# Optimization experiments

Measured on AMD Instinct MI355X. Metric: run time of the kernel, lower is better.

## Reference

```python
import jax, jax.numpy as jnp
import numpy as np

EPS = 1e-08
SINKHORN_ITERS = 5
SINKHORN_TAU = 0.05


def l2_normalize(x, axis=-1):
    return x / (jnp.linalg.norm(x, axis=axis, keepdims=True) + EPS)


def sinkhorn_balanced(logits, iters=SINKHORN_ITERS, tau=SINKHORN_TAU):
    # logits: [B, N, K]
    b, n, k = logits.shape
    q = jnp.exp(logits / tau)
    q = q / (jnp.sum(q, axis=(1, 2), keepdims=True) + EPS)
    target_row = 1.0 / float(n)
    target_col = 1.0 / float(k)
    for _ in range(iters):
        q = q / (jnp.sum(q, axis=2, keepdims=True) + EPS) * target_row
        q = q / (jnp.sum(q, axis=1, keepdims=True) + EPS) * target_col
    q = q / (jnp.sum(q, axis=2, keepdims=True) + EPS)
    return q


def assign(x, proto):
    x_n = l2_normalize(x)          # [B,N,D]
    p_n = l2_normalize(proto)      # [K,D]
    sim = jnp.einsum('bnd,kd->bnk', x_n, p_n)
    a = sinkhorn_balanced(sim)
    z_rec = jnp.einsum('bnk,kd->bnd', a, p_n)
    return z_rec, a, sim


def setup_inputs() -> dict:
    key = jax.random.key(0)
    k1, k2, k3, k4 = jax.random.split(key, 4)
    B, N, D, K = 16, 1024, 256, 256
    return {
        'f_rgb': jax.random.normal(k1, (B, N, D), dtype=jnp.float32),
        'f_sn': jax.random.normal(k2, (B, N, D), dtype=jnp.float32),
        'proto_rgb': jax.random.normal(k3, (K, D), dtype=jnp.float32) * 0.02,
        'proto_sn': jax.random.normal(k4, (K, D), dtype=jnp.float32) * 0.02,
    }


def reference(f_rgb, f_sn, proto_rgb, proto_sn):
    z_rgb, assign_rgb, sim_rgb = assign(f_rgb, proto_rgb)
    z_sn, assign_sn, sim_sn = assign(f_sn, proto_sn)
    # cross-modal consistency maps: [B,N,N]
    rgb_to_sn = jnp.matmul(assign_rgb, jnp.swapaxes(assign_sn, -1, -2))
    sn_to_rgb = jnp.matmul(assign_sn, jnp.swapaxes(assign_rgb, -1, -2))
    sem_consistency = 0.5 * (
        1.0 - jnp.clip(jnp.mean(rgb_to_sn), 0.0, 1.0)
        + 1.0 - jnp.clip(jnp.mean(sn_to_rgb), 0.0, 1.0)
    )
    return (z_rgb, z_sn, assign_rgb, assign_sn, sim_rgb, sim_sn, sem_consistency)
```

## Files before the change

### kernel.cpp

```cpp
#include <hip/hip_runtime.h>
#include <hip/hip_bf16.h>
#include <cstdint>
#include <cstddef>

#define EPS 1e-8f

typedef __attribute__((ext_vector_type(8))) short short8;
typedef __attribute__((ext_vector_type(4))) float floatx4;

static constexpr int Bb = 16, Nn = 1024, Dd = 256, Kk = 256;
static constexpr int M = Bb * Nn;
static constexpr size_t PM = (size_t)M * 256;

static constexpr size_t OUT_Z      = 0;
static constexpr size_t OUT_ASSIGN = 2 * PM;
static constexpr size_t OUT_SIM    = 4 * PM;
static constexpr size_t OUT_SEM    = 6 * PM;

static constexpr size_t OFF_XN  = 0;
static constexpr size_t OFF_QB  = 16777216;
static constexpr size_t OFF_PN  = 33554432;
static constexpr size_t OFF_PNT = 33816576;
static constexpr size_t OFF_U   = 34078720;
static constexpr size_t OFF_T   = 34209792;
static constexpr size_t OFF_SC  = 34209920;
static constexpr size_t OFF_CS  = 34406528;
static constexpr size_t ZERO_OFF = OFF_T;
static constexpr size_t ZERO_SZ  = 128 + 196608 + 32768;
static constexpr int    NZ_FLOATS = (int)(ZERO_SZ / 4);

__device__ __forceinline__ unsigned short f2bf(float f) {
    unsigned int b = __float_as_uint(f);
    b += 0x7fffu + ((b >> 16) & 1u);
    return (unsigned short)(b >> 16);
}
__device__ __forceinline__ float bf2f(unsigned short u) {
    return __uint_as_float(((unsigned int)u) << 16);
}

typedef const __attribute__((address_space(1))) unsigned int* gas_u32p;
typedef __attribute__((address_space(3))) unsigned int* las_u32p;
__device__ __forceinline__ void lds_cp16(const unsigned short* g, short* l) {
    __builtin_amdgcn_global_load_lds((gas_u32p)g, (las_u32p)l, 16, 0, 0);
}

__global__ __launch_bounds__(256) void prep_kernel(const float* __restrict__ fr,
                                                   const float* __restrict__ fs,
                                                   unsigned short* __restrict__ xn) {
    int mod = blockIdx.y;
    int row = blockIdx.x * 4 + (threadIdx.x >> 6);
    int lane = threadIdx.x & 63;
    const float* src = (mod ? fs : fr) + (size_t)row * 256;
    float4 v = ((const float4*)src)[lane];
    float ss = v.x * v.x + v.y * v.y + v.z * v.z + v.w * v.w;
    #pragma unroll
    for (int m = 1; m < 64; m <<= 1) ss += __shfl_xor(ss, m);
    float sc = 1.0f / (sqrtf(ss) + EPS);
    ushort4 u4;
    u4.x = f2bf(v.x * sc); u4.y = f2bf(v.y * sc);
    u4.z = f2bf(v.z * sc); u4.w = f2bf(v.w * sc);
    *(ushort4*)(xn + (size_t)mod * PM + (size_t)row * 256 + lane * 4) = u4;
}

__global__ __launch_bounds__(64) void proto_kernel(const float* __restrict__ pr,
                                                   const float* __restrict__ ps,
                                                   unsigned short* __restrict__ pn,
                                                   unsigned short* __restrict__ pnt,
                                                   float* __restrict__ zp) {
    int gid = blockIdx.x * 64 + threadIdx.x;
    for (int i = gid; i < NZ_FLOATS; i += 32768) zp[i] = 0.f;

    int row = blockIdx.x & 255;
    int mod = blockIdx.x >> 8;
    const float* p = (mod ? ps : pr) + (size_t)row * 256;
    int lane = threadIdx.x;
    float4 v = ((const float4*)p)[lane];
    float ss = v.x * v.x + v.y * v.y + v.z * v.z + v.w * v.w;
    #pragma unroll
    for (int m = 1; m < 64; m <<= 1) ss += __shfl_xor(ss, m);
    float sc = 1.0f / (sqrtf(ss) + EPS);
    ushort4 u4;
    u4.x = f2bf(v.x * sc); u4.y = f2bf(v.y * sc);
    u4.z = f2bf(v.z * sc); u4.w = f2bf(v.w * sc);
    *(ushort4*)(pn + (size_t)mod * 65536 + (size_t)row * 256 + lane * 4) = u4;
    unsigned short* pt = pnt + (size_t)mod * 65536 + row;
    pt[(size_t)(lane * 4 + 0) * 256] = u4.x;
    pt[(size_t)(lane * 4 + 1) * 256] = u4.y;
    pt[(size_t)(lane * 4 + 2) * 256] = u4.z;
    pt[(size_t)(lane * 4 + 3) * 256] = u4.w;
}

template <int MODE>
__global__ __launch_bounds__(256) void gemm_kernel(const unsigned short* __restrict__ Asrc,
                                                   const unsigned short* __restrict__ Bsrc,
                                                   unsigned short* __restrict__ qb,
                                                   float* __restrict__ doutf,
                                                   float* __restrict__ Tg) {
    __shared__ short Al[8192];
    __shared__ short Bl[8192];

    int bx = blockIdx.x;
    int by = blockIdx.y;
    int mod = blockIdx.z;
    int t = threadIdx.x;
    int lane = t & 63, wv = t >> 6;
    int wrow = (wv >> 1) * 64, wcol = (wv & 1) * 64;
    int g = lane >> 4, ml = lane & 15;

    const unsigned short* A0 = Asrc + (size_t)mod * PM + (size_t)by * 128 * 256;
    const unsigned short* B0 = Bsrc + (size_t)mod * 65536 + (size_t)bx * 128 * 256;

    floatx4 acc[4][4];
    #pragma unroll
    for (int i = 0; i < 4; i++)
        #pragma unroll
        for (int j = 0; j < 4; j++) acc[i][j] = (floatx4){0.f, 0.f, 0.f, 0.f};

    for (int kh = 0; kh < 4; kh++) {
        #pragma unroll
        for (int i = 0; i < 4; i++) {
            int sI = i * 256 + t;
            int r = sI >> 3, cs = sI & 7;
            int cg = cs ^ (r & 7);
            size_t goff = (size_t)r * 256 + kh * 64 + cg * 8;
            lds_cp16(A0 + goff, &Al[sI * 8]);
            lds_cp16(B0 + goff, &Bl[sI * 8]);
        }
        __syncthreads();
        #pragma unroll
        for (int ks = 0; ks < 2; ks++) {
            short8 af[4], bfr[4];
            int c = ks * 4 + g;
            #pragma unroll
            for (int mt = 0; mt < 4; mt++) {
                int row = wrow + mt * 16 + ml;
                af[mt] = *(const short8*)&Al[row * 64 + (c ^ (row & 7)) * 8];
            }
            #pragma unroll
            for (int nt = 0; nt < 4; nt++) {
                int row = wcol + nt * 16 + ml;
                bfr[nt] = *(const short8*)&Bl[row * 64 + (c ^ (row & 7)) * 8];
            }
            #pragma unroll
            for (int mt = 0; mt < 4; mt++)
                #pragma unroll
                for (int nt = 0; nt < 4; nt++)
                    acc[mt][nt] = __builtin_amdgcn_mfma_f32_16x16x32_bf16(af[mt], bfr[nt], acc[mt][nt], 0, 0, 0);
        }
        __syncthreads();
    }

    int g4 = g << 2;
    float tsum = 0.f;
    #pragma unroll
    for (int mt = 0; mt < 4; mt++)
        #pragma unroll
        for (int nt = 0; nt < 4; nt++)
            #pragma unroll
            for (int reg = 0; reg < 4; reg++) {
                float s = acc[mt][nt][reg];
                int row = by * 128 + wrow + mt * 16 + g4 + reg;
                int col = bx * 128 + wcol + nt * 16 + ml;
                size_t idx = (size_t)row * 256 + col;
                if (MODE == 0) {
                    doutf[OUT_SIM + (size_t)mod * PM + idx] = s;
                    unsigned short eb = f2bf(__expf(s * 20.0f));
                    qb[(size_t)mod * PM + idx] = eb;
                    tsum += bf2f(eb);
                } else {
                    doutf[OUT_Z + (size_t)mod * PM + idx] = s;
                }
            }
    if (MODE == 0) {
        #pragma unroll
        for (int mk = 1; mk < 64; mk <<= 1) tsum += __shfl_xor(tsum, mk);
        if (lane == 0) atomicAdd(&Tg[mod * 16 + (by >> 3)], tsum);
    }
}

__global__ __launch_bounds__(256) void pass_kernel(const unsigned short* __restrict__ qbg,
                                                   float* __restrict__ u,
                                                   const float* __restrict__ Tg,
                                                   float* __restrict__ Sc,
                                                   float* __restrict__ cs,
                                                   float* __restrict__ doutf,
                                                   unsigned short* __restrict__ abf,
                                                   int pass) {
    __shared__ float vcur[256];
    __shared__ float unl[32];
    __shared__ float wsum[4][256];
    int tile = blockIdx.x, b = blockIdx.y, mod = blockIdx.z;
    int t = threadIdx.x;
    {
        float v = 1.0f;
        for (int j = 1; j < pass; j++) {
            float sc = Sc[((size_t)(mod * 6 + j) * 16 + b) * 256 + t];
            v = v * (1.0f / 256.0f) / (v * sc + EPS);
        }
        vcur[t] = v;
    }
    __syncthreads();

    int r = t >> 3, q = t & 7;
    size_t row = (size_t)b * 1024 + tile * 32 + r;
    const unsigned short* qrow = qbg + ((size_t)mod * M + row) * 256;
    const short8* q8 = (const short8*)(qrow + q * 32);
    const float4* v4 = (const float4*)(vcur + q * 32);
    float sr = 0.f;
    #pragma unroll
    for (int i = 0; i < 4; i++) {
        short8 qv = q8[i];
        float4 va = v4[2 * i], vb = v4[2 * i + 1];
        sr += bf2f((unsigned short)qv[0]) * va.x + bf2f((unsigned short)qv[1]) * va.y
            + bf2f((unsigned short)qv[2]) * va.z + bf2f((unsigned short)qv[3]) * va.w
            + bf2f((unsigned short)qv[4]) * vb.x + bf2f((unsigned short)qv[5]) * vb.y
            + bf2f((unsigned short)qv[6]) * vb.z + bf2f((unsigned short)qv[7]) * vb.w;
    }
    sr += __shfl_xor(sr, 1);
    sr += __shfl_xor(sr, 2);
    sr += __shfl_xor(sr, 4);

    float up = (pass == 1) ? 1.0f / (Tg[mod * 16 + b] + EPS) : u[(size_t)mod * M + row];
    float un;
    if (pass <= 5) un = up * (1.0f / 1024.0f) / (up * sr + EPS);
    else           un = up / (up * sr + EPS);
    if (q == 0) {
        if (pass <= 5) u[(size_t)mod * M + row] = un;
        unl[r] = un;
    }
    __syncthreads();

    int wv = t >> 6, lane = t & 63;
    float c0 = 0.f, c1 = 0.f, c2 = 0.f, c3 = 0.f;
    float4 vv = *(const float4*)(vcur + lane * 4);
    size_t rowbase = (size_t)mod * M + (size_t)b * 1024 + tile * 32;
    if (pass <= 5) {
        #pragma unroll
        for (int rr8 = 0; rr8 < 8; rr8++) {
            int rr = wv * 8 + rr8;
            float unr = unl[rr];
            ushort4 qv = *(const ushort4*)(qbg + (rowbase + rr) * 256 + lane * 4);
            c0 += bf2f(qv.x) * unr;
            c1 += bf2f(qv.y) * unr;
            c2 += bf2f(qv.z) * unr;
            c3 += bf2f(qv.w) * unr;
        }
    } else {
        float* aout = doutf + OUT_ASSIGN + (size_t)mod * PM;
        unsigned short* ab = abf + (size_t)mod * PM;
        #pragma unroll
        for (int rr8 = 0; rr8 < 8; rr8++) {
            int rr = wv * 8 + rr8;
            float unr = unl[rr];
            size_t ro = ((size_t)b * 1024 + tile * 32 + rr) * 256;
            ushort4 qv = *(const ushort4*)(qbg + (rowbase + rr) * 256 + lane * 4);
            float4 a = make_float4(bf2f(qv.x) * unr * vv.x, bf2f(qv.y) * unr * vv.y,
                                   bf2f(qv.z) * unr * vv.z, bf2f(qv.w) * unr * vv.w);
            *(float4*)(aout + ro + lane * 4) = a;
            ushort4 o;
            o.x = f2bf(a.x); o.y = f2bf(a.y); o.z = f2bf(a.z); o.w = f2bf(a.w);
            *(ushort4*)(ab + ro + lane * 4) = o;
            c0 += a.x; c1 += a.y; c2 += a.z; c3 += a.w;
        }
    }
    *(float4*)&wsum[wv][lane * 4] = make_float4(c0, c1, c2, c3);
    __syncthreads();
    {
        float ssum = wsum[0][t] + wsum[1][t] + wsum[2][t] + wsum[3][t];
        float* dst = (pass <= 5) ? &Sc[((size_t)(mod * 6 + pass) * 16 + b) * 256 + t]
                                 : &cs[((size_t)mod * 16 + b) * 256 + t];
        atomicAdd(dst, ssum);
    }
}

__global__ __launch_bounds__(256) void sem_kernel(const float* __restrict__ cs,
                                                  float* __restrict__ doutf) {
    int t = threadIdx.x;
    float s = 0.f;
    #pragma unroll
    for (int b = 0; b < 16; b++)
        s += cs[b * 256 + t] * cs[4096 + b * 256 + t];
    #pragma unroll
    for (int mk = 1; mk < 64; mk <<= 1) s += __shfl_xor(s, mk);
    __shared__ float red[4];
    if ((t & 63) == 0) red[t >> 6] = s;
    __syncthreads();
    if (t == 0) {
        float tot = red[0] + red[1] + red[2] + red[3];
        float mv = tot / 16777216.0f;
        mv = fminf(fmaxf(mv, 0.f), 1.f);
        doutf[OUT_SEM] = 1.0f - mv;
    }
}

extern "C" void kernel_launch(void* const* d_in, const int* in_sizes, int n_in,
                              void* d_out, int out_size, void* d_ws, size_t ws_size,
                              hipStream_t stream) {
    const float* f_rgb = (const float*)d_in[0];
    const float* f_sn  = (const float*)d_in[1];
    const float* p_rgb = (const float*)d_in[2];
    const float* p_sn  = (const float*)d_in[3];
    char* ws = (char*)d_ws;
    unsigned short* xn   = (unsigned short*)(ws + OFF_XN);
    unsigned short* abf  = (unsigned short*)(ws + OFF_XN);
    unsigned short* qb   = (unsigned short*)(ws + OFF_QB);
    unsigned short* pn   = (unsigned short*)(ws + OFF_PN);
    unsigned short* pnt  = (unsigned short*)(ws + OFF_PNT);
    float* u             = (float*)(ws + OFF_U);
    float* Tg            = (float*)(ws + OFF_T);
    float* Sc            = (float*)(ws + OFF_SC);
    float* cs            = (float*)(ws + OFF_CS);
    float* doutf         = (float*)d_out;

    proto_kernel<<<dim3(512), 64, 0, stream>>>(p_rgb, p_sn, pn, pnt, (float*)(ws + ZERO_OFF));
    prep_kernel<<<dim3(4096, 2), 256, 0, stream>>>(f_rgb, f_sn, xn);
    gemm_kernel<0><<<dim3(2, 128, 2), 256, 0, stream>>>(xn, pn, qb, doutf, Tg);
    for (int p = 1; p <= 6; p++)
        pass_kernel<<<dim3(32, 16, 2), 256, 0, stream>>>(qb, u, Tg, Sc, cs, doutf, abf, p);
    gemm_kernel<1><<<dim3(2, 128, 2), 256, 0, stream>>>(abf, pnt, qb, doutf, Tg);
    sem_kernel<<<1, 256, 0, stream>>>(cs, doutf);
}
```

Before: 211.0 us.

## Fuse six Sinkhorn pass launches into one persistent kernel with LDS-resident tiles

Replaces the six per-iteration Sinkhorn launches with one kernel of 512 blocks. Each block loads its 64-row bf16 tile of q into LDS once and keeps the row scalings in registers. Column sums are exchanged between the 16 blocks of a batch through atomics and a spin-wait counter per iteration. This removes launch overhead and the repeated global re-reads of q. The cost is a cross-block barrier that depends on every block being co-resident, more shared memory per block, and a shuffle-heavy column reduction.

```diff
diff --git a/kernel.cpp b/kernel.cpp
--- a/kernel.cpp
+++ b/kernel.cpp
@@ -25,8 +25,9 @@
 static constexpr size_t OFF_T   = 34209792;
 static constexpr size_t OFF_SC  = 34209920;
 static constexpr size_t OFF_CS  = 34406528;
+static constexpr size_t OFF_CTR = 34439296;
 static constexpr size_t ZERO_OFF = OFF_T;
-static constexpr size_t ZERO_SZ  = 128 + 196608 + 32768;
+static constexpr size_t ZERO_SZ  = 128 + 196608 + 32768 + 1024;
 static constexpr int    NZ_FLOATS = (int)(ZERO_SZ / 4);
 
 __device__ __forceinline__ unsigned short f2bf(float f) {
@@ -178,98 +179,130 @@
     }
 }
 
-__global__ __launch_bounds__(256) void pass_kernel(const unsigned short* __restrict__ qbg,
-                                                   float* __restrict__ u,
-                                                   const float* __restrict__ Tg,
-                                                   float* __restrict__ Sc,
-                                                   float* __restrict__ cs,
-                                                   float* __restrict__ doutf,
-                                                   unsigned short* __restrict__ abf,
-                                                   int pass) {
+__global__ __launch_bounds__(256) void sinkhorn_kernel(const unsigned short* __restrict__ qbg,
+                                                       const float* __restrict__ Tg,
+                                                       float* __restrict__ Sc,
+                                                       int* __restrict__ ctr,
+                                                       float* __restrict__ cs,
+                                                       float* __restrict__ doutf,
+                                                       unsigned short* __restrict__ abf) {
+    __shared__ unsigned short q0t[64 * 264];
     __shared__ float vcur[256];
-    __shared__ float unl[32];
-    __shared__ float wsum[4][256];
+    __shared__ float unl[64];
+    __shared__ float wacc[4][256];
+
     int tile = blockIdx.x, b = blockIdx.y, mod = blockIdx.z;
+    int grp = mod * 16 + b;
     int t = threadIdx.x;
+    int wv = t >> 6, lane = t & 63;
+
+    size_t rowbase = (size_t)b * 1024 + (size_t)tile * 64;
+    const unsigned short* gsrc = qbg + ((size_t)mod * M + rowbase) * 256;
+
+    #pragma unroll
+    for (int it = 0; it < 8; it++) {
+        int idx = it * 256 + t;
+        int r = idx >> 5, c = idx & 31;
+        short8 v = *(const short8*)(gsrc + (size_t)r * 256 + c * 8);
+        *(short8*)&q0t[r * 264 + c * 8] = v;
+    }
+    vcur[t] = 1.0f;
+    float vpriv = 1.0f;
+    __syncthreads();
+
+    int r = t >> 2, q = t & 3;
+    float uown = 0.f;
+    const float uinit = 1.0f / (Tg[grp] + EPS);
+
+    for (int p = 1; p <= 5; p++) {
+        short8 st[8];
+        float sr = 0.f;
+        #pragma unroll
+        for (int i = 0; i < 8; i++) {
+            st[i] = *(const short8*)&q0t[r * 264 + q * 64 + i * 8];
+            const float* vv = &vcur[q * 64 + i * 8];
+            sr += bf2f((unsigned short)st[i][0]) * vv[0] + bf2f((unsigned short)st[i][1]) * vv[1]
+                + bf2f((unsigned short)st[i][2]) * vv[2] + bf2f((unsigned short)st[i][3]) * vv[3]
+                + bf2f((unsigned short)st[i][4]) * vv[4] + bf2f((unsigned short)st[i][5]) * vv[5]
+                + bf2f((unsigned short)st[i][6]) * vv[6] + bf2f((unsigned short)st[i][7]) * vv[7];
+        }
+        sr += __shfl_xor(sr, 1);
+        sr += __shfl_xor(sr, 2);
+        float up = (p == 1) ? uinit : uown;
+        uown = up * (1.0f / 1024.0f) / (up * sr + EPS);
+
+        #pragma unroll
+        for (int i = 0; i < 64; i++) {
+            float prod = bf2f((unsigned short)st[i >> 3][i & 7]) * uown;
+            prod += __shfl_xor(prod, 4);
+            prod += __shfl_xor(prod, 8);
+            prod += __shfl_xor(prod, 16);
+            prod += __shfl_xor(prod, 32);
+            if (lane < 4) wacc[wv][lane * 64 + i] = prod;
+        }
+        __syncthreads();
+        float ssum = wacc[0][t] + wacc[1][t] + wacc[2][t] + wacc[3][t];
+        atomicAdd(&Sc[((size_t)(p - 1) * 32 + grp) * 256 + t], ssum);
+        __syncthreads();
+
+        if (t == 0) {
+            __threadfence();
+            atomicAdd(&ctr[(p - 1) * 32 + grp], 1);
+            while (__hip_atomic_load(&ctr[(p - 1) * 32 + grp],
+                                     __ATOMIC_ACQUIRE, __HIP_MEMORY_SCOPE_AGENT) < 16)
+                __builtin_amdgcn_s_sleep(4);
+            __threadfence();
+        }
+        __syncthreads();
+
+        float sc = __hip_atomic_load(&Sc[((size_t)(p - 1) * 32 + grp) * 256 + t],
+                                     __ATOMIC_RELAXED, __HIP_MEMORY_SCOPE_AGENT);
+        vpriv = vpriv * (1.0f / 256.0f) / (vpriv * sc + EPS);
+        vcur[t] = vpriv;
+        __syncthreads();
+    }
+
     {
-        float v = 1.0f;
-        for (int j = 1; j < pass; j++) {
-            float sc = Sc[((size_t)(mod * 6 + j) * 16 + b) * 256 + t];
-            v = v * (1.0f / 256.0f) / (v * sc + EPS);
-        }
-        vcur[t] = v;
+        float sr = 0.f;
+        #pragma unroll
+        for (int i = 0; i < 8; i++) {
+            short8 sv = *(const short8*)&q0t[r * 264 + q * 64 + i * 8];
+            const float* vv = &vcur[q * 64 + i * 8];
+            sr += bf2f((unsigned short)sv[0]) * vv[0] + bf2f((unsigned short)sv[1]) * vv[1]
+                + bf2f((unsigned short)sv[2]) * vv[2] + bf2f((unsigned short)sv[3]) * vv[3]
+                + bf2f((unsigned short)sv[4]) * vv[4] + bf2f((unsigned short)sv[5]) * vv[5]
+                + bf2f((unsigned short)sv[6]) * vv[6] + bf2f((unsigned short)sv[7]) * vv[7];
+        }
+        sr += __shfl_xor(sr, 1);
+        sr += __shfl_xor(sr, 2);
+        float uf = uown / (uown * sr + EPS);
+        if (q == 0) unl[r] = uf;
     }
     __syncthreads();
 
-    int r = t >> 3, q = t & 7;
-    size_t row = (size_t)b * 1024 + tile * 32 + r;
-    const unsigned short* qrow = qbg + ((size_t)mod * M + row) * 256;
-    const short8* q8 = (const short8*)(qrow + q * 32);
-    const float4* v4 = (const float4*)(vcur + q * 32);
-    float sr = 0.f;
-    #pragma unroll
-    for (int i = 0; i < 4; i++) {
-        short8 qv = q8[i];
-        float4 va = v4[2 * i], vb = v4[2 * i + 1];
-        sr += bf2f((unsigned short)qv[0]) * va.x + bf2f((unsigned short)qv[1]) * va.y
-            + bf2f((unsigned short)qv[2]) * va.z + bf2f((unsigned short)qv[3]) * va.w
-            + bf2f((unsigned short)qv[4]) * vb.x + bf2f((unsigned short)qv[5]) * vb.y
-            + bf2f((unsigned short)qv[6]) * vb.z + bf2f((unsigned short)qv[7]) * vb.w;
-    }
-    sr += __shfl_xor(sr, 1);
-    sr += __shfl_xor(sr, 2);
-    sr += __shfl_xor(sr, 4);
-
-    float up = (pass == 1) ? 1.0f / (Tg[mod * 16 + b] + EPS) : u[(size_t)mod * M + row];
-    float un;
-    if (pass <= 5) un = up * (1.0f / 1024.0f) / (up * sr + EPS);
-    else           un = up / (up * sr + EPS);
-    if (q == 0) {
-        if (pass <= 5) u[(size_t)mod * M + row] = un;
-        unl[r] = un;
-    }
-    __syncthreads();
-
-    int wv = t >> 6, lane = t & 63;
+    float* aout = doutf + OUT_ASSIGN + (size_t)mod * PM;
+    unsigned short* ab = abf + (size_t)mod * PM;
+    float4 vv4 = *(const float4*)&vcur[lane * 4];
     float c0 = 0.f, c1 = 0.f, c2 = 0.f, c3 = 0.f;
-    float4 vv = *(const float4*)(vcur + lane * 4);
-    size_t rowbase = (size_t)mod * M + (size_t)b * 1024 + tile * 32;
-    if (pass <= 5) {
-        #pragma unroll
-        for (int rr8 = 0; rr8 < 8; rr8++) {
-            int rr = wv * 8 + rr8;
-            float unr = unl[rr];
-            ushort4 qv = *(const ushort4*)(qbg + (rowbase + rr) * 256 + lane * 4);
-            c0 += bf2f(qv.x) * unr;
-            c1 += bf2f(qv.y) * unr;
-            c2 += bf2f(qv.z) * unr;
-            c3 += bf2f(qv.w) * unr;
-        }
-    } else {
-        float* aout = doutf + OUT_ASSIGN + (size_t)mod * PM;
-        unsigned short* ab = abf + (size_t)mod * PM;
-        #pragma unroll
-        for (int rr8 = 0; rr8 < 8; rr8++) {
-            int rr = wv * 8 + rr8;
-            float unr = unl[rr];
-            size_t ro = ((size_t)b * 1024 + tile * 32 + rr) * 256;
-            ushort4 qv = *(const ushort4*)(qbg + (rowbase + rr) * 256 + lane * 4);
-            float4 a = make_float4(bf2f(qv.x) * unr * vv.x, bf2f(qv.y) * unr * vv.y,
-                                   bf2f(qv.z) * unr * vv.z, bf2f(qv.w) * unr * vv.w);
-            *(float4*)(aout + ro + lane * 4) = a;
-            ushort4 o;
-            o.x = f2bf(a.x); o.y = f2bf(a.y); o.z = f2bf(a.z); o.w = f2bf(a.w);
-            *(ushort4*)(ab + ro + lane * 4) = o;
-            c0 += a.x; c1 += a.y; c2 += a.z; c3 += a.w;
-        }
-    }
-    *(float4*)&wsum[wv][lane * 4] = make_float4(c0, c1, c2, c3);
+    #pragma unroll
+    for (int rr = 0; rr < 16; rr++) {
+        int row = wv * 16 + rr;
+        float ur = unl[row];
+        ushort4 qv = *(const ushort4*)&q0t[row * 264 + lane * 4];
+        float4 a = make_float4(bf2f(qv.x) * ur * vv4.x, bf2f(qv.y) * ur * vv4.y,
+                               bf2f(qv.z) * ur * vv4.z, bf2f(qv.w) * ur * vv4.w);
+        size_t ro = (rowbase + row) * 256;
+        *(float4*)(aout + ro + lane * 4) = a;
+        ushort4 o;
+        o.x = f2bf(a.x); o.y = f2bf(a.y); o.z = f2bf(a.z); o.w = f2bf(a.w);
+        *(ushort4*)(ab + ro + lane * 4) = o;
+        c0 += a.x; c1 += a.y; c2 += a.z; c3 += a.w;
+    }
+    *(float4*)&wacc[wv][lane * 4] = make_float4(c0, c1, c2, c3);
     __syncthreads();
     {
-        float ssum = wsum[0][t] + wsum[1][t] + wsum[2][t] + wsum[3][t];
-        float* dst = (pass <= 5) ? &Sc[((size_t)(mod * 6 + pass) * 16 + b) * 256 + t]
-                                 : &cs[((size_t)mod * 16 + b) * 256 + t];
-        atomicAdd(dst, ssum);
+        float ssum = wacc[0][t] + wacc[1][t] + wacc[2][t] + wacc[3][t];
+        atomicAdd(&cs[(size_t)grp * 256 + t], ssum);
     }
 }
 
@@ -306,17 +339,16 @@
     unsigned short* qb   = (unsigned short*)(ws + OFF_QB);
     unsigned short* pn   = (unsigned short*)(ws + OFF_PN);
     unsigned short* pnt  = (unsigned short*)(ws + OFF_PNT);
-    float* u             = (float*)(ws + OFF_U);
     float* Tg            = (float*)(ws + OFF_T);
     float* Sc            = (float*)(ws + OFF_SC);
     float* cs            = (float*)(ws + OFF_CS);
+    int*   ctr           = (int*)(ws + OFF_CTR);
     float* doutf         = (float*)d_out;
 
     proto_kernel<<<dim3(512), 64, 0, stream>>>(p_rgb, p_sn, pn, pnt, (float*)(ws + ZERO_OFF));
     prep_kernel<<<dim3(4096, 2), 256, 0, stream>>>(f_rgb, f_sn, xn);
     gemm_kernel<0><<<dim3(2, 128, 2), 256, 0, stream>>>(xn, pn, qb, doutf, Tg);
-    for (int p = 1; p <= 6; p++)
-        pass_kernel<<<dim3(32, 16, 2), 256, 0, stream>>>(qb, u, Tg, Sc, cs, doutf, abf, p);
+    sinkhorn_kernel<<<dim3(16, 16, 2), 256, 0, stream>>>(qb, Tg, Sc, ctr, cs, doutf, abf);
     gemm_kernel<1><<<dim3(2, 128, 2), 256, 0, stream>>>(abf, pnt, qb, doutf, Tg);
     sem_kernel<<<1, 256, 0, stream>>>(cs, doutf);
 }
```

Result: slower. 420.2 us (+99.1%).
